# Optimization experiments

Measured on AMD Instinct MI355X. Metric: run time of the kernel, lower is better.

The kernel has to match this reference:

```python
import jax, jax.numpy as jnp
import numpy as np

N = 50000      # nodes
E = 1600000    # edges (before self loops)
B = 512        # graphs
D = 128        # gcn dim (constant across the 3 GAT layers)
H = 1024       # hidden_dim
O = 128        # output_dim
NEG_SLOPE = 0.2


def setup_inputs() -> dict:
    key = jax.random.key(0)
    ks = jax.random.split(key, 24)
    inp = {
        "x": jax.random.normal(ks[0], (N, D), jnp.float32),
        "edge_index": jax.random.randint(ks[1], (2, E), 0, N, dtype=jnp.int64),
        "edge_weight": jax.random.uniform(ks[2], (E,), jnp.float32),
        "batch": jnp.sort(jax.random.randint(ks[3], (N,), 0, B, dtype=jnp.int64)),
    }
    s = 1.0 / np.sqrt(D)
    for i in range(3):
        k = 4 + 4 * i
        inp[f"W{i+1}"] = jax.random.normal(ks[k], (D, D), jnp.float32) * s
        inp[f"as{i+1}"] = jax.random.normal(ks[k + 1], (D,), jnp.float32) * s
        inp[f"ad{i+1}"] = jax.random.normal(ks[k + 2], (D,), jnp.float32) * s
        inp[f"b{i+1}"] = jnp.zeros((D,), jnp.float32)
    inp["Wf1"] = jax.random.normal(ks[16], (D, H), jnp.float32) * s
    inp["bf1"] = jnp.zeros((H,), jnp.float32)
    inp["Wf2"] = jax.random.normal(ks[17], (H, O), jnp.float32) * (1.0 / np.sqrt(H))
    inp["bf2"] = jnp.zeros((O,), jnp.float32)
    return inp


def gat_conv(x, src, dst, W, a_src, a_dst, b):
    """PyG GATConv, heads=1: gather -> leakyrelu -> segment softmax -> scatter-add."""
    h = x @ W                                   # [N, D]
    e = jax.nn.leaky_relu(jnp.take(h @ a_src, src) + jnp.take(h @ a_dst, dst), NEG_SLOPE)  # [E']
    m = jax.ops.segment_max(e, dst, num_segments=N)
    ex = jnp.exp(e - m[dst])
    denom = jax.ops.segment_sum(ex, dst, num_segments=N)
    alpha = ex / denom[dst]                      # segment softmax over incoming edges
    out = jax.ops.segment_sum(alpha[:, None] * h[src], dst, num_segments=N)
    return out + b


def reference(x, edge_index, edge_weight, batch,
              W1, as1, ad1, b1, W2, as2, ad2, b2, W3, as3, ad3, b3,
              Wf1, bf1, Wf2, bf2):
    # GATConv adds self loops; edge_weight is unused by GATConv (faithful to original)
    loop = jnp.arange(N, dtype=edge_index.dtype)
    src = jnp.concatenate([edge_index[0], loop])
    dst = jnp.concatenate([edge_index[1], loop])

    h = gat_conv(x, src, dst, W1, as1, ad1, b1)
    h = jax.nn.relu(gat_conv(h, src, dst, W2, as2, ad2, b2))
    h = jax.nn.relu(gat_conv(h, src, dst, W3, as3, ad3, b3))

    # global mean pool (gep)
    sums = jax.ops.segment_sum(h, batch, num_segments=B)        # [B, D]
    counts = jax.ops.segment_sum(jnp.ones((N,), h.dtype), batch, num_segments=B)
    pooled = sums / jnp.maximum(counts, 1.0)[:, None]

    # MLP head; dropout is identity at inference
    o = jax.nn.relu(pooled) @ Wf1 + bf1
    o = jax.nn.relu(o) @ Wf2 + bf2
    return o
```

## Files before the change

### kernel.cpp

```cpp
#include <hip/hip_runtime.h>
#include <cstdint>
#include <cstddef>

#define NEG_SLOPE 0.2f

typedef _Float16 f16x8 __attribute__((ext_vector_type(8)));
typedef float f32x4v __attribute__((ext_vector_type(4)));

__device__ __forceinline__ unsigned enc_f(float f) {
  unsigned u = __float_as_uint(f);
  return (u & 0x80000000u) ? ~u : (u | 0x80000000u);
}
__device__ __forceinline__ float dec_f(unsigned u) {
  return (u & 0x80000000u) ? __uint_as_float(u ^ 0x80000000u) : __uint_as_float(~u);
}

#define AST 136
#define WST 136
#define HST 132
#define SMEM_BYTES (64 * AST * 2 + 128 * WST * 2)

__global__ void k_bounds(const int* __restrict__ batch, int N, int B,
                         int* __restrict__ gstart, unsigned* __restrict__ maxPart) {
  int n = blockIdx.x * blockDim.x + threadIdx.x;
  if (n < 768) maxPart[n] = 0u;
  if (n >= N) return;
  int cur = batch[n];
  if (n == 0) {
    for (int g = 0; g <= cur; g++) gstart[g] = 0;
  } else {
    int prev = batch[n - 1];
    for (int g = prev + 1; g <= cur; g++) gstart[g] = n;
  }
  if (n == N - 1) {
    for (int g = cur + 1; g <= B; g++) gstart[g] = N;
  }
}

__global__ void k_count_rank(const int* __restrict__ dst, int E,
                             int* counts, int* __restrict__ rank) {
  int e = blockIdx.x * blockDim.x + threadIdx.x;
  if (e < E) rank[e] = atomicAdd(&counts[dst[e]], 1);
}

__global__ __launch_bounds__(1024) void k_scan1(const int* __restrict__ counts, int N,
                                                int* __restrict__ row_ptr, int* __restrict__ part) {
  __shared__ int tmp[1024];
  int t = threadIdx.x;
  int i = blockIdx.x * 1024 + t;
  int v = (i < N) ? 1 + counts[i] : 0;
  tmp[t] = v;
  __syncthreads();
  for (int off = 1; off < 1024; off <<= 1) {
    int u = (t >= off) ? tmp[t - off] : 0;
    __syncthreads();
    tmp[t] += u;
    __syncthreads();
  }
  if (i < N) row_ptr[i + 1] = tmp[t];
  if (t == 1023) part[blockIdx.x] = tmp[t];
}

__global__ __launch_bounds__(1024) void k_scan3(int* __restrict__ row_ptr,
                                                const int* __restrict__ part, int N) {
  __shared__ int s_off;
  int bi = blockIdx.x;
  if (threadIdx.x == 0) {
    int run = 0;
    for (int b = 0; b < bi; b++) run += part[b];
    s_off = run;
    if (bi == 0) row_ptr[0] = 0;
  }
  __syncthreads();
  int i = bi * 1024 + threadIdx.x;
  if (i < N) row_ptr[i + 1] += s_off;
}

__global__ void k_fill(const int* __restrict__ src, const int* __restrict__ dst,
                       const int* __restrict__ rank, int E, int N,
                       const int* __restrict__ row_ptr, int* __restrict__ col) {
  int i = blockIdx.x * blockDim.x + threadIdx.x;
  if (i < N) col[row_ptr[i]] = i;
  int e = i - N;
  if (e >= 0 && e < E) col[row_ptr[dst[e]] + 1 + rank[e]] = src[e];
}

__global__ __launch_bounds__(256) void k_gemm_fused(const float* __restrict__ A32,
                                                    const unsigned short* __restrict__ A16,
                                                    const float* __restrict__ W,
                                                    unsigned short* __restrict__ hb,
                                                    const float* __restrict__ asrc,
                                                    const float* __restrict__ adst,
                                                    float* __restrict__ sv, float* __restrict__ dv,
                                                    unsigned* __restrict__ maxSlot, int M) {
  __shared__ __align__(16) char smem[SMEM_BYTES];
  __shared__ float redmax[4];
  _Float16* Ah = (_Float16*)smem;
  _Float16* Wt = (_Float16*)(smem + 64 * AST * 2);
  float*    hS = (float*)(smem + 64 * AST * 2);
  int t = threadIdx.x;
  int rowbase = blockIdx.x * 64;

  if (A16) {
    for (int i = t; i < 64 * 16; i += 256) {
      int r = i >> 4, c8 = (i & 15) << 3;
      int gr = rowbase + r;
      uint4 v = make_uint4(0u, 0u, 0u, 0u);
      if (gr < M) v = *(const uint4*)&A16[(size_t)gr * 128 + c8];
      *(uint4*)&Ah[r * AST + c8] = v;
    }
  } else {
    for (int i = t; i < 64 * 32; i += 256) {
      int r = i >> 5, c4 = (i & 31) << 2;
      int gr = rowbase + r;
      float4 v = make_float4(0.f, 0.f, 0.f, 0.f);
      if (gr < M) v = *(const float4*)&A32[(size_t)gr * 128 + c4];
      _Float16 tmp[4] = {(_Float16)v.x, (_Float16)v.y, (_Float16)v.z, (_Float16)v.w};
      *(short4*)&Ah[r * AST + c4] = *(short4*)tmp;
    }
  }
  for (int i = t; i < 128 * 32; i += 256) {
    int r = i >> 5, c4 = (i & 31) << 2;
    float4 v = *(const float4*)&W[(size_t)r * 128 + c4];
    Wt[(c4 + 0) * WST + r] = (_Float16)v.x;
    Wt[(c4 + 1) * WST + r] = (_Float16)v.y;
    Wt[(c4 + 2) * WST + r] = (_Float16)v.z;
    Wt[(c4 + 3) * WST + r] = (_Float16)v.w;
  }
  __syncthreads();

  int wave = t >> 6, lane = t & 63, quad = lane >> 4, l15 = lane & 15;
  f32x4v acc[4][2];
#pragma unroll
  for (int mt = 0; mt < 4; mt++)
#pragma unroll
    for (int nt = 0; nt < 2; nt++) {
      acc[mt][nt][0] = 0.f; acc[mt][nt][1] = 0.f; acc[mt][nt][2] = 0.f; acc[mt][nt][3] = 0.f;
    }

#pragma unroll
  for (int s = 0; s < 4; s++) {
    int k0 = (s << 5) + (quad << 3);
    f16x8 af[4], bf[2];
#pragma unroll
    for (int mt = 0; mt < 4; mt++)
      af[mt] = *(f16x8*)&Ah[(mt * 16 + l15) * AST + k0];
#pragma unroll
    for (int nt = 0; nt < 2; nt++)
      bf[nt] = *(f16x8*)&Wt[(wave * 32 + nt * 16 + l15) * WST + k0];
#pragma unroll
    for (int mt = 0; mt < 4; mt++)
#pragma unroll
      for (int nt = 0; nt < 2; nt++)
        acc[mt][nt] = __builtin_amdgcn_mfma_f32_16x16x32_f16(af[mt], bf[nt], acc[mt][nt], 0, 0, 0);
  }
  __syncthreads();

#pragma unroll
  for (int mt = 0; mt < 4; mt++)
#pragma unroll
    for (int nt = 0; nt < 2; nt++)
#pragma unroll
      for (int rr = 0; rr < 4; rr++)
        hS[(mt * 16 + quad * 4 + rr) * HST + wave * 32 + nt * 16 + l15] = acc[mt][nt][rr];
  __syncthreads();

  int tx = t & 31, ty = t >> 5;
  float4 av  = *(const float4*)&asrc[tx * 4];
  float4 adv = *(const float4*)&adst[tx * 4];
  float wmax = -1e30f;
#pragma unroll
  for (int r8 = 0; r8 < 8; r8++) {
    int row = r8 * 8 + ty;
    int gr = rowbase + row;
    float4 hv = *(float4*)&hS[row * HST + tx * 4];
    float ps = hv.x * av.x + hv.y * av.y + hv.z * av.z + hv.w * av.w;
    float pd = hv.x * adv.x + hv.y * adv.y + hv.z * adv.z + hv.w * adv.w;
#pragma unroll
    for (int mask = 16; mask; mask >>= 1) {
      ps += __shfl_xor(ps, mask);
      pd += __shfl_xor(pd, mask);
    }
    if (gr < M) {
      _Float16 hq[4] = {(_Float16)hv.x, (_Float16)hv.y, (_Float16)hv.z, (_Float16)hv.w};
      *(uint2*)&hb[(size_t)gr * 128 + tx * 4] = *(uint2*)hq;
      if (tx == 0) { sv[gr] = ps; dv[gr] = pd; wmax = fmaxf(wmax, ps); }
    }
  }
#pragma unroll
  for (int mask = 32; mask; mask >>= 1) wmax = fmaxf(wmax, __shfl_xor(wmax, mask));
  if ((t & 63) == 0) redmax[t >> 6] = wmax;
  __syncthreads();
  if (t == 0) {
    float mx = fmaxf(fmaxf(redmax[0], redmax[1]), fmaxf(redmax[2], redmax[3]));
    atomicMax(&maxSlot[blockIdx.x & 255], enc_f(mx));
  }
}

__global__ __launch_bounds__(256) void k_agg(const unsigned short* __restrict__ hb,
                                             const float* __restrict__ sv,
                                             const float* __restrict__ dv,
                                             const int* __restrict__ row_ptr,
                                             const int* __restrict__ col,
                                             const float* __restrict__ bias,
                                             const unsigned* __restrict__ maxSlot,
                                             unsigned short* __restrict__ out16,
                                             int N, int relu) {
  int wid = (int)((blockIdx.x * (size_t)blockDim.x + threadIdx.x) >> 6);
  int lane = threadIdx.x & 63;
  if (wid >= N) return;

  unsigned mp = max(max(maxSlot[lane], maxSlot[lane + 64]),
                    max(maxSlot[lane + 128], maxSlot[lane + 192]));
#pragma unroll
  for (int off = 32; off; off >>= 1) mp = max(mp, __shfl_xor(mp, off));
  float maxS = dec_f(mp);

  int beg = row_ptr[wid], end = row_ptr[wid + 1];
  float dn = dv[wid];
  float m = maxS + dn;
  m = (m > 0.f) ? m : NEG_SLOPE * m;

  int g = lane >> 4, sub = lane & 15;
  const uint32_t* hbu = (const uint32_t*)hb;
  float acc[8];
#pragma unroll
  for (int k = 0; k < 8; k++) acc[k] = 0.f;
  float dsum = 0.f;

  int j = beg + g;
  float wc = 0.f;
  uint4 hc = make_uint4(0u, 0u, 0u, 0u);
  if (j < end) {
    int sn = col[j];
    float e = sv[sn] + dn;
    e = (e > 0.f) ? e : NEG_SLOPE * e;
    wc = __expf(e - m);
    hc = *(const uint4*)(hbu + (size_t)sn * 64 + sub * 4);
  }
  j += 4;
  while (j < end) {
    int sn = col[j];
    float e = sv[sn] + dn;
    e = (e > 0.f) ? e : NEG_SLOPE * e;
    float wn = __expf(e - m);
    uint4 hn = *(const uint4*)(hbu + (size_t)sn * 64 + sub * 4);
    dsum += wc;
    const _Float16* hp = (const _Float16*)&hc;
#pragma unroll
    for (int k = 0; k < 8; k++) acc[k] += wc * (float)hp[k];
    wc = wn; hc = hn;
    j += 4;
  }
  {
    dsum += wc;
    const _Float16* hp = (const _Float16*)&hc;
#pragma unroll
    for (int k = 0; k < 8; k++) acc[k] += wc * (float)hp[k];
  }

  dsum += __shfl_xor(dsum, 16);
  dsum += __shfl_xor(dsum, 32);
#pragma unroll
  for (int k = 0; k < 8; k++) {
    acc[k] += __shfl_xor(acc[k], 16);
    acc[k] += __shfl_xor(acc[k], 32);
  }
  if (lane < 16) {
    float inv = 1.f / dsum;
    float o[8];
    const float* bp = &bias[sub * 8];
#pragma unroll
    for (int k = 0; k < 8; k++) {
      o[k] = acc[k] * inv + bp[k];
      if (relu) o[k] = fmaxf(o[k], 0.f);
    }
    _Float16 q[8];
#pragma unroll
    for (int k = 0; k < 8; k++) q[k] = (_Float16)o[k];
    *(uint4*)&out16[(size_t)wid * 128 + sub * 8] = *(uint4*)q;
  }
}

__global__ __launch_bounds__(64) void k_pool(const unsigned short* __restrict__ h16,
                                             const int* __restrict__ gstart,
                                             float* __restrict__ pooled, int B) {
  int b = blockIdx.x, c = threadIdx.x;
  int s0 = gstart[b], s1 = gstart[b + 1];
  const uint32_t* hu = (const uint32_t*)h16;
  float a0 = 0.f, a1 = 0.f;
  for (int n = s0; n < s1; n++) {
    union { uint32_t u; _Float16 h[2]; } cv;
    cv.u = hu[(size_t)n * 64 + c];
    a0 += (float)cv.h[0];
    a1 += (float)cv.h[1];
  }
  int cnt = s1 - s0;
  float inv = 1.f / (float)(cnt > 0 ? cnt : 1);
  pooled[b * 128 + 2 * c]     = fmaxf(a0 * inv, 0.f);
  pooled[b * 128 + 2 * c + 1] = fmaxf(a1 * inv, 0.f);
}

__global__ __launch_bounds__(256) void k_mlp(const float* __restrict__ pooled,
                                             const float* __restrict__ Wf1,
                                             const float* __restrict__ bf1,
                                             const float* __restrict__ Wf2,
                                             const float* __restrict__ bf2,
                                             float* __restrict__ out, int B) {
  __shared__ float P[4][128];
  __shared__ float H1[4][1024];
  __shared__ float R[4][128];
  int t = threadIdx.x;
  int g0 = blockIdx.x * 4;

  for (int i = t; i < 4 * 128; i += 256) {
    int gi = i >> 7, c = i & 127;
    P[gi][c] = (g0 + gi < B) ? pooled[(size_t)(g0 + gi) * 128 + c] : 0.f;
  }
  __syncthreads();

#pragma unroll
  for (int cb = 0; cb < 4; cb++) {
    int c = cb * 256 + t;
    float a0 = 0.f, a1 = 0.f, a2 = 0.f, a3 = 0.f;
    for (int k = 0; k < 128; k++) {
      float w = Wf1[(size_t)k * 1024 + c];
      a0 += P[0][k] * w; a1 += P[1][k] * w; a2 += P[2][k] * w; a3 += P[3][k] * w;
    }
    float b = bf1[c];
    H1[0][c] = fmaxf(a0 + b, 0.f);
    H1[1][c] = fmaxf(a1 + b, 0.f);
    H1[2][c] = fmaxf(a2 + b, 0.f);
    H1[3][c] = fmaxf(a3 + b, 0.f);
  }
  __syncthreads();

  int c = t & 127, hh = t >> 7;
  float a0 = 0.f, a1 = 0.f, a2 = 0.f, a3 = 0.f;
  int k0 = hh * 512;
  for (int k = k0; k < k0 + 512; k++) {
    float w = Wf2[(size_t)k * 128 + c];
    a0 += H1[0][k] * w; a1 += H1[1][k] * w; a2 += H1[2][k] * w; a3 += H1[3][k] * w;
  }
  if (hh == 1) { R[0][c] = a0; R[1][c] = a1; R[2][c] = a2; R[3][c] = a3; }
  __syncthreads();
  if (hh == 0) {
    float b = bf2[c];
    float o0 = a0 + R[0][c] + b;
    float o1 = a1 + R[1][c] + b;
    float o2 = a2 + R[2][c] + b;
    float o3 = a3 + R[3][c] + b;
    if (g0 + 0 < B) out[(size_t)(g0 + 0) * 128 + c] = o0;
    if (g0 + 1 < B) out[(size_t)(g0 + 1) * 128 + c] = o1;
    if (g0 + 2 < B) out[(size_t)(g0 + 2) * 128 + c] = o2;
    if (g0 + 3 < B) out[(size_t)(g0 + 3) * 128 + c] = o3;
  }
}

extern "C" void kernel_launch(void* const* d_in, const int* in_sizes, int n_in,
                              void* d_out, int out_size, void* d_ws, size_t ws_size,
                              hipStream_t stream) {
  const float* x     = (const float*)d_in[0];
  const int*   ei    = (const int*)d_in[1];
  const int*   batch = (const int*)d_in[3];
  const float* W1 = (const float*)d_in[4];
  const float* as1 = (const float*)d_in[5];
  const float* ad1 = (const float*)d_in[6];
  const float* b1 = (const float*)d_in[7];
  const float* W2 = (const float*)d_in[8];
  const float* as2 = (const float*)d_in[9];
  const float* ad2 = (const float*)d_in[10];
  const float* b2 = (const float*)d_in[11];
  const float* W3 = (const float*)d_in[12];
  const float* as3 = (const float*)d_in[13];
  const float* ad3 = (const float*)d_in[14];
  const float* b3 = (const float*)d_in[15];
  const float* Wf1 = (const float*)d_in[16];
  const float* bf1 = (const float*)d_in[17];
  const float* Wf2 = (const float*)d_in[18];
  const float* bf2 = (const float*)d_in[19];

  const int N = in_sizes[0] / 128;
  const int E = in_sizes[1] / 2;
  const int B = out_size / 128;

  char* base_ws = (char*)d_ws;
  size_t off = 0;
  auto carve = [&](size_t bytes) -> void* {
    off = (off + 255) & ~(size_t)255;
    void* p = base_ws + off;
    off += bytes;
    return p;
  };
  int* counts   = (int*)carve((size_t)N * 4);
  int* row_ptr  = (int*)carve((size_t)(N + 1) * 4);
  int* rank     = (int*)carve((size_t)E * 4);
  int* col      = (int*)carve((size_t)(E + N) * 4);
  int* part     = (int*)carve(1024 * 4);
  int* gstart   = (int*)carve((size_t)(B + 1) * 4);
  unsigned* maxPart = (unsigned*)carve(768 * 4);
  float* sbuf   = (float*)carve((size_t)N * 4);
  float* dbuf   = (float*)carve((size_t)N * 4);
  unsigned short* hb  = (unsigned short*)carve((size_t)N * 128 * 2);
  unsigned short* a16 = (unsigned short*)carve((size_t)N * 128 * 2);
  float* pooled = (float*)carve((size_t)B * 128 * 4);

  const int* srcp = ei;
  const int* dstp = ei + E;
  const int nb = (N + 1023) / 1024;
  const int Gg = (N + 63) / 64;

  hipMemsetAsync(counts, 0, (size_t)N * 4, stream);
  hipLaunchKernelGGL(k_bounds, dim3((N + 255) / 256), dim3(256), 0, stream,
                     batch, N, B, gstart, maxPart);
  hipLaunchKernelGGL(k_count_rank, dim3((E + 255) / 256), dim3(256), 0, stream,
                     dstp, E, counts, rank);
  hipLaunchKernelGGL(k_scan1, dim3(nb), dim3(1024), 0, stream, counts, N, row_ptr, part);
  hipLaunchKernelGGL(k_scan3, dim3(nb), dim3(1024), 0, stream, row_ptr, part, N);
  hipLaunchKernelGGL(k_fill, dim3((E + N + 255) / 256), dim3(256), 0, stream,
                     srcp, dstp, rank, E, N, row_ptr, col);

  hipLaunchKernelGGL(k_gemm_fused, dim3(Gg), dim3(256), 0, stream,
                     x, (const unsigned short*)nullptr, W1, hb, as1, ad1,
                     sbuf, dbuf, maxPart + 0 * 256, N);
  hipLaunchKernelGGL(k_agg, dim3((N + 3) / 4), dim3(256), 0, stream,
                     hb, sbuf, dbuf, row_ptr, col, b1, maxPart + 0 * 256, a16, N, 0);

  hipLaunchKernelGGL(k_gemm_fused, dim3(Gg), dim3(256), 0, stream,
                     (const float*)nullptr, a16, W2, hb, as2, ad2,
                     sbuf, dbuf, maxPart + 1 * 256, N);
  hipLaunchKernelGGL(k_agg, dim3((N + 3) / 4), dim3(256), 0, stream,
                     hb, sbuf, dbuf, row_ptr, col, b2, maxPart + 1 * 256, a16, N, 1);

  hipLaunchKernelGGL(k_gemm_fused, dim3(Gg), dim3(256), 0, stream,
                     (const float*)nullptr, a16, W3, hb, as3, ad3,
                     sbuf, dbuf, maxPart + 2 * 256, N);
  hipLaunchKernelGGL(k_agg, dim3((N + 3) / 4), dim3(256), 0, stream,
                     hb, sbuf, dbuf, row_ptr, col, b3, maxPart + 2 * 256, a16, N, 1);

  hipLaunchKernelGGL(k_pool, dim3(B), dim3(64), 0, stream, a16, gstart, pooled, B);
  hipLaunchKernelGGL(k_mlp, dim3((B + 3) / 4), dim3(256), 0, stream,
                     pooled, Wf1, bf1, Wf2, bf2, (float*)d_out, B);
}
```

Measured before the change: 558.2 us.

## Fuse CSR fill with first GEMM, fold count memset, parallelize pooling

Merges the CSR column fill and the layer-1 projection GEMM into one launch, interleaving one GEMM block among every nine blocks so the two independent workloads overlap. The zeroing of per-node counts moves into the bounds kernel, which removes a separate memset. The pooling kernel now uses four waves per graph that each sum a slice of the nodes, then combines them through shared memory. Together these cut launch count and serialization, at the cost of the fused kernel carrying the GEMM's large shared-memory allocation even for fill blocks, which may lower occupancy for the fill work.

```diff
diff --git a/kernel.cpp b/kernel.cpp
--- a/kernel.cpp
+++ b/kernel.cpp
@@ -21,10 +21,12 @@
 #define SMEM_BYTES (64 * AST * 2 + 128 * WST * 2)
 
 __global__ void k_bounds(const int* __restrict__ batch, int N, int B,
-                         int* __restrict__ gstart, unsigned* __restrict__ maxPart) {
+                         int* __restrict__ gstart, unsigned* __restrict__ maxPart,
+                         int* __restrict__ counts) {
   int n = blockIdx.x * blockDim.x + threadIdx.x;
   if (n < 768) maxPart[n] = 0u;
   if (n >= N) return;
+  counts[n] = 0;
   int cur = batch[n];
   if (n == 0) {
     for (int g = 0; g <= cur; g++) gstart[g] = 0;
@@ -76,17 +78,146 @@
   if (i < N) row_ptr[i + 1] += s_off;
 }
 
-__global__ void k_fill(const int* __restrict__ src, const int* __restrict__ dst,
-                       const int* __restrict__ rank, int E, int N,
-                       const int* __restrict__ row_ptr, int* __restrict__ col) {
-  int i = blockIdx.x * blockDim.x + threadIdx.x;
-  if (i < N) col[row_ptr[i]] = i;
-  int e = i - N;
-  if (e >= 0 && e < E) col[row_ptr[dst[e]] + 1 + rank[e]] = src[e];
-}
-
-__global__ __launch_bounds__(256) void k_gemm_fused(const float* __restrict__ A32,
-                                                    const unsigned short* __restrict__ A16,
+__device__ __forceinline__ void gemm_body(char* smem, float* redmax, int bx,
+                                          const float* __restrict__ A32,
+                                          const unsigned short* __restrict__ A16,
+                                          const float* __restrict__ W,
+                                          unsigned short* __restrict__ hb,
+                                          const float* __restrict__ asrc,
+                                          const float* __restrict__ adst,
+                                          float* __restrict__ sv, float* __restrict__ dv,
+                                          unsigned* __restrict__ maxSlot, int M) {
+  _Float16* Ah = (_Float16*)smem;
+  _Float16* Wt = (_Float16*)(smem + 64 * AST * 2);
+  float*    hS = (float*)(smem + 64 * AST * 2);
+  int t = threadIdx.x;
+  int rowbase = bx * 64;
+
+  if (A16) {
+    for (int i = t; i < 64 * 16; i += 256) {
+      int r = i >> 4, c8 = (i & 15) << 3;
+      int gr = rowbase + r;
+      uint4 v = make_uint4(0u, 0u, 0u, 0u);
+      if (gr < M) v = *(const uint4*)&A16[(size_t)gr * 128 + c8];
+      *(uint4*)&Ah[r * AST + c8] = v;
+    }
+  } else {
+    for (int i = t; i < 64 * 32; i += 256) {
+      int r = i >> 5, c4 = (i & 31) << 2;
+      int gr = rowbase + r;
+      float4 v = make_float4(0.f, 0.f, 0.f, 0.f);
+      if (gr < M) v = *(const float4*)&A32[(size_t)gr * 128 + c4];
+      _Float16 tmp[4] = {(_Float16)v.x, (_Float16)v.y, (_Float16)v.z, (_Float16)v.w};
+      *(short4*)&Ah[r * AST + c4] = *(short4*)tmp;
+    }
+  }
+  for (int i = t; i < 128 * 32; i += 256) {
+    int r = i >> 5, c4 = (i & 31) << 2;
+    float4 v = *(const float4*)&W[(size_t)r * 128 + c4];
+    Wt[(c4 + 0) * WST + r] = (_Float16)v.x;
+    Wt[(c4 + 1) * WST + r] = (_Float16)v.y;
+    Wt[(c4 + 2) * WST + r] = (_Float16)v.z;
+    Wt[(c4 + 3) * WST + r] = (_Float16)v.w;
+  }
+  __syncthreads();
+
+  int wave = t >> 6, lane = t & 63, quad = lane >> 4, l15 = lane & 15;
+  f32x4v acc[4][2];
+#pragma unroll
+  for (int mt = 0; mt < 4; mt++)
+#pragma unroll
+    for (int nt = 0; nt < 2; nt++) {
+      acc[mt][nt][0] = 0.f; acc[mt][nt][1] = 0.f; acc[mt][nt][2] = 0.f; acc[mt][nt][3] = 0.f;
+    }
+
+#pragma unroll
+  for (int s = 0; s < 4; s++) {
+    int k0 = (s << 5) + (quad << 3);
+    f16x8 af[4], bf[2];
+#pragma unroll
+    for (int mt = 0; mt < 4; mt++)
+      af[mt] = *(f16x8*)&Ah[(mt * 16 + l15) * AST + k0];
+#pragma unroll
+    for (int nt = 0; nt < 2; nt++)
+      bf[nt] = *(f16x8*)&Wt[(wave * 32 + nt * 16 + l15) * WST + k0];
+#pragma unroll
+    for (int mt = 0; mt < 4; mt++)
+#pragma unroll
+      for (int nt = 0; nt < 2; nt++)
+        acc[mt][nt] = __builtin_amdgcn_mfma_f32_16x16x32_f16(af[mt], bf[nt], acc[mt][nt], 0, 0, 0);
+  }
+  __syncthreads();
+
+#pragma unroll
+  for (int mt = 0; mt < 4; mt++)
+#pragma unroll
+    for (int nt = 0; nt < 2; nt++)
+#pragma unroll
+      for (int rr = 0; rr < 4; rr++)
+        hS[(mt * 16 + quad * 4 + rr) * HST + wave * 32 + nt * 16 + l15] = acc[mt][nt][rr];
+  __syncthreads();
+
+  int tx = t & 31, ty = t >> 5;
+  float4 av  = *(const float4*)&asrc[tx * 4];
+  float4 adv = *(const float4*)&adst[tx * 4];
+  float wmax = -1e30f;
+#pragma unroll
+  for (int r8 = 0; r8 < 8; r8++) {
+    int row = r8 * 8 + ty;
+    int gr = rowbase + row;
+    float4 hv = *(float4*)&hS[row * HST + tx * 4];
+    float ps = hv.x * av.x + hv.y * av.y + hv.z * av.z + hv.w * av.w;
+    float pd = hv.x * adv.x + hv.y * adv.y + hv.z * adv.z + hv.w * adv.w;
+#pragma unroll
+    for (int mask = 16; mask; mask >>= 1) {
+      ps += __shfl_xor(ps, mask);
+      pd += __shfl_xor(pd, mask);
+    }
+    if (gr < M) {
+      _Float16 hq[4] = {(_Float16)hv.x, (_Float16)hv.y, (_Float16)hv.z, (_Float16)hv.w};
+      *(uint2*)&hb[(size_t)gr * 128 + tx * 4] = *(uint2*)hq;
+      if (tx == 0) { sv[gr] = ps; dv[gr] = pd; wmax = fmaxf(wmax, ps); }
+    }
+  }
+#pragma unroll
+  for (int mask = 32; mask; mask >>= 1) wmax = fmaxf(wmax, __shfl_xor(wmax, mask));
+  if ((t & 63) == 0) redmax[t >> 6] = wmax;
+  __syncthreads();
+  if (t == 0) {
+    float mx = fmaxf(fmaxf(redmax[0], redmax[1]), fmaxf(redmax[2], redmax[3]));
+    atomicMax(&maxSlot[bx & 255], enc_f(mx));
+  }
+}
+
+__global__ __launch_bounds__(256) void k_fill_gemm(const int* __restrict__ src,
+                                                   const int* __restrict__ dst,
+                                                   const int* __restrict__ rank, int E, int N,
+                                                   const int* __restrict__ row_ptr,
+                                                   int* __restrict__ col,
+                                                   const float* __restrict__ A32,
+                                                   const float* __restrict__ W,
+                                                   unsigned short* __restrict__ hb,
+                                                   const float* __restrict__ asrc,
+                                                   const float* __restrict__ adst,
+                                                   float* __restrict__ sv, float* __restrict__ dv,
+                                                   unsigned* __restrict__ maxSlot, int Gg) {
+  __shared__ __align__(16) char smem[SMEM_BYTES];
+  __shared__ float redmax[4];
+  int b = (int)blockIdx.x;
+  bool isGemm = ((b % 9) == 4) && ((b / 9) < Gg);
+  if (isGemm) {
+    gemm_body(smem, redmax, b / 9, A32, (const unsigned short*)nullptr, W,
+              hb, asrc, adst, sv, dv, maxSlot, N);
+  } else {
+    int nGemmBefore = (b >= 4) ? min((b - 4) / 9 + 1, Gg) : 0;
+    int i = (b - nGemmBefore) * 256 + threadIdx.x;
+    if (i < N) col[row_ptr[i]] = i;
+    int e = i - N;
+    if (e >= 0 && e < E) col[row_ptr[dst[e]] + 1 + rank[e]] = src[e];
+  }
+}
+
+__global__ __launch_bounds__(256) void k_gemm_fused(const unsigned short* __restrict__ A16,
                                                     const float* __restrict__ W,
                                                     unsigned short* __restrict__ hb,
                                                     const float* __restrict__ asrc,
@@ -95,106 +226,8 @@
                                                     unsigned* __restrict__ maxSlot, int M) {
   __shared__ __align__(16) char smem[SMEM_BYTES];
   __shared__ float redmax[4];
-  _Float16* Ah = (_Float16*)smem;
-  _Float16* Wt = (_Float16*)(smem + 64 * AST * 2);
-  float*    hS = (float*)(smem + 64 * AST * 2);
-  int t = threadIdx.x;
-  int rowbase = blockIdx.x * 64;
-
-  if (A16) {
-    for (int i = t; i < 64 * 16; i += 256) {
-      int r = i >> 4, c8 = (i & 15) << 3;
-      int gr = rowbase + r;
-      uint4 v = make_uint4(0u, 0u, 0u, 0u);
-      if (gr < M) v = *(const uint4*)&A16[(size_t)gr * 128 + c8];
-      *(uint4*)&Ah[r * AST + c8] = v;
-    }
-  } else {
-    for (int i = t; i < 64 * 32; i += 256) {
-      int r = i >> 5, c4 = (i & 31) << 2;
-      int gr = rowbase + r;
-      float4 v = make_float4(0.f, 0.f, 0.f, 0.f);
-      if (gr < M) v = *(const float4*)&A32[(size_t)gr * 128 + c4];
-      _Float16 tmp[4] = {(_Float16)v.x, (_Float16)v.y, (_Float16)v.z, (_Float16)v.w};
-      *(short4*)&Ah[r * AST + c4] = *(short4*)tmp;
-    }
-  }
-  for (int i = t; i < 128 * 32; i += 256) {
-    int r = i >> 5, c4 = (i & 31) << 2;
-    float4 v = *(const float4*)&W[(size_t)r * 128 + c4];
-    Wt[(c4 + 0) * WST + r] = (_Float16)v.x;
-    Wt[(c4 + 1) * WST + r] = (_Float16)v.y;
-    Wt[(c4 + 2) * WST + r] = (_Float16)v.z;
-    Wt[(c4 + 3) * WST + r] = (_Float16)v.w;
-  }
-  __syncthreads();
-
-  int wave = t >> 6, lane = t & 63, quad = lane >> 4, l15 = lane & 15;
-  f32x4v acc[4][2];
-#pragma unroll
-  for (int mt = 0; mt < 4; mt++)
-#pragma unroll
-    for (int nt = 0; nt < 2; nt++) {
-      acc[mt][nt][0] = 0.f; acc[mt][nt][1] = 0.f; acc[mt][nt][2] = 0.f; acc[mt][nt][3] = 0.f;
-    }
-
-#pragma unroll
-  for (int s = 0; s < 4; s++) {
-    int k0 = (s << 5) + (quad << 3);
-    f16x8 af[4], bf[2];
-#pragma unroll
-    for (int mt = 0; mt < 4; mt++)
-      af[mt] = *(f16x8*)&Ah[(mt * 16 + l15) * AST + k0];
-#pragma unroll
-    for (int nt = 0; nt < 2; nt++)
-      bf[nt] = *(f16x8*)&Wt[(wave * 32 + nt * 16 + l15) * WST + k0];
-#pragma unroll
-    for (int mt = 0; mt < 4; mt++)
-#pragma unroll
-      for (int nt = 0; nt < 2; nt++)
-        acc[mt][nt] = __builtin_amdgcn_mfma_f32_16x16x32_f16(af[mt], bf[nt], acc[mt][nt], 0, 0, 0);
-  }
-  __syncthreads();
-
-#pragma unroll
-  for (int mt = 0; mt < 4; mt++)
-#pragma unroll
-    for (int nt = 0; nt < 2; nt++)
-#pragma unroll
-      for (int rr = 0; rr < 4; rr++)
-        hS[(mt * 16 + quad * 4 + rr) * HST + wave * 32 + nt * 16 + l15] = acc[mt][nt][rr];
-  __syncthreads();
-
-  int tx = t & 31, ty = t >> 5;
-  float4 av  = *(const float4*)&asrc[tx * 4];
-  float4 adv = *(const float4*)&adst[tx * 4];
-  float wmax = -1e30f;
-#pragma unroll
-  for (int r8 = 0; r8 < 8; r8++) {
-    int row = r8 * 8 + ty;
-    int gr = rowbase + row;
-    float4 hv = *(float4*)&hS[row * HST + tx * 4];
-    float ps = hv.x * av.x + hv.y * av.y + hv.z * av.z + hv.w * av.w;
-    float pd = hv.x * adv.x + hv.y * adv.y + hv.z * adv.z + hv.w * adv.w;
-#pragma unroll
-    for (int mask = 16; mask; mask >>= 1) {
-      ps += __shfl_xor(ps, mask);
-      pd += __shfl_xor(pd, mask);
-    }
-    if (gr < M) {
-      _Float16 hq[4] = {(_Float16)hv.x, (_Float16)hv.y, (_Float16)hv.z, (_Float16)hv.w};
-      *(uint2*)&hb[(size_t)gr * 128 + tx * 4] = *(uint2*)hq;
-      if (tx == 0) { sv[gr] = ps; dv[gr] = pd; wmax = fmaxf(wmax, ps); }
-    }
-  }
-#pragma unroll
-  for (int mask = 32; mask; mask >>= 1) wmax = fmaxf(wmax, __shfl_xor(wmax, mask));
-  if ((t & 63) == 0) redmax[t >> 6] = wmax;
-  __syncthreads();
-  if (t == 0) {
-    float mx = fmaxf(fmaxf(redmax[0], redmax[1]), fmaxf(redmax[2], redmax[3]));
-    atomicMax(&maxSlot[blockIdx.x & 255], enc_f(mx));
-  }
+  gemm_body(smem, redmax, (int)blockIdx.x, (const float*)nullptr, A16, W,
+            hb, asrc, adst, sv, dv, maxSlot, M);
 }
 
 __global__ __launch_bounds__(256) void k_agg(const unsigned short* __restrict__ hb,
@@ -282,23 +315,34 @@
   }
 }
 
-__global__ __launch_bounds__(64) void k_pool(const unsigned short* __restrict__ h16,
-                                             const int* __restrict__ gstart,
-                                             float* __restrict__ pooled, int B) {
-  int b = blockIdx.x, c = threadIdx.x;
+__global__ __launch_bounds__(256) void k_pool(const unsigned short* __restrict__ h16,
+                                              const int* __restrict__ gstart,
+                                              float* __restrict__ pooled, int B) {
+  __shared__ float red[4][128];
+  int b = blockIdx.x, t = threadIdx.x;
+  int c = t & 63, seg = t >> 6;
   int s0 = gstart[b], s1 = gstart[b + 1];
+  int cnt = s1 - s0;
+  int per = (cnt + 3) >> 2;
+  int n0 = s0 + seg * per;
+  int n1 = min(n0 + per, s1);
   const uint32_t* hu = (const uint32_t*)h16;
   float a0 = 0.f, a1 = 0.f;
-  for (int n = s0; n < s1; n++) {
+  for (int n = n0; n < n1; n++) {
     union { uint32_t u; _Float16 h[2]; } cv;
     cv.u = hu[(size_t)n * 64 + c];
     a0 += (float)cv.h[0];
     a1 += (float)cv.h[1];
   }
-  int cnt = s1 - s0;
-  float inv = 1.f / (float)(cnt > 0 ? cnt : 1);
-  pooled[b * 128 + 2 * c]     = fmaxf(a0 * inv, 0.f);
-  pooled[b * 128 + 2 * c + 1] = fmaxf(a1 * inv, 0.f);
+  if (seg) { red[seg][2 * c] = a0; red[seg][2 * c + 1] = a1; }
+  __syncthreads();
+  if (seg == 0) {
+    a0 += red[1][2 * c] + red[2][2 * c] + red[3][2 * c];
+    a1 += red[1][2 * c + 1] + red[2][2 * c + 1] + red[3][2 * c + 1];
+    float inv = 1.f / (float)(cnt > 0 ? cnt : 1);
+    pooled[b * 128 + 2 * c]     = fmaxf(a0 * inv, 0.f);
+    pooled[b * 128 + 2 * c + 1] = fmaxf(a1 * inv, 0.f);
+  }
 }
 
 __global__ __launch_bounds__(256) void k_mlp(const float* __restrict__ pooled,
@@ -409,36 +453,33 @@
   const int* dstp = ei + E;
   const int nb = (N + 1023) / 1024;
   const int Gg = (N + 63) / 64;
-
-  hipMemsetAsync(counts, 0, (size_t)N * 4, stream);
+  const int Gf = (E + N + 255) / 256;
+
   hipLaunchKernelGGL(k_bounds, dim3((N + 255) / 256), dim3(256), 0, stream,
-                     batch, N, B, gstart, maxPart);
+                     batch, N, B, gstart, maxPart, counts);
   hipLaunchKernelGGL(k_count_rank, dim3((E + 255) / 256), dim3(256), 0, stream,
                      dstp, E, counts, rank);
   hipLaunchKernelGGL(k_scan1, dim3(nb), dim3(1024), 0, stream, counts, N, row_ptr, part);
   hipLaunchKernelGGL(k_scan3, dim3(nb), dim3(1024), 0, stream, row_ptr, part, N);
-  hipLaunchKernelGGL(k_fill, dim3((E + N + 255) / 256), dim3(256), 0, stream,
-                     srcp, dstp, rank, E, N, row_ptr, col);
-
-  hipLaunchKernelGGL(k_gemm_fused, dim3(Gg), dim3(256), 0, stream,
-                     x, (const unsigned short*)nullptr, W1, hb, as1, ad1,
-                     sbuf, dbuf, maxPart + 0 * 256, N);
+
+  hipLaunchKernelGGL(k_fill_gemm, dim3(Gf + Gg), dim3(256), 0, stream,
+                     srcp, dstp, rank, E, N, row_ptr, col,
+                     x, W1, hb, as1, ad1, sbuf, dbuf, maxPart + 0 * 256, Gg);
+
   hipLaunchKernelGGL(k_agg, dim3((N + 3) / 4), dim3(256), 0, stream,
                      hb, sbuf, dbuf, row_ptr, col, b1, maxPart + 0 * 256, a16, N, 0);
 
   hipLaunchKernelGGL(k_gemm_fused, dim3(Gg), dim3(256), 0, stream,
-                     (const float*)nullptr, a16, W2, hb, as2, ad2,
-                     sbuf, dbuf, maxPart + 1 * 256, N);
+                     a16, W2, hb, as2, ad2, sbuf, dbuf, maxPart + 1 * 256, N);
   hipLaunchKernelGGL(k_agg, dim3((N + 3) / 4), dim3(256), 0, stream,
                      hb, sbuf, dbuf, row_ptr, col, b2, maxPart + 1 * 256, a16, N, 1);
 
   hipLaunchKernelGGL(k_gemm_fused, dim3(Gg), dim3(256), 0, stream,
-                     (const float*)nullptr, a16, W3, hb, as3, ad3,
-                     sbuf, dbuf, maxPart + 2 * 256, N);
+                     a16, W3, hb, as3, ad3, sbuf, dbuf, maxPart + 2 * 256, N);
   hipLaunchKernelGGL(k_agg, dim3((N + 3) / 4), dim3(256), 0, stream,
                      hb, sbuf, dbuf, row_ptr, col, b3, maxPart + 2 * 256, a16, N, 1);
 
-  hipLaunchKernelGGL(k_pool, dim3(B), dim3(64), 0, stream, a16, gstart, pooled, B);
+  hipLaunchKernelGGL(k_pool, dim3(B), dim3(256), 0, stream, a16, gstart, pooled, B);
   hipLaunchKernelGGL(k_mlp, dim3((B + 3) / 4), dim3(256), 0, stream,
                      pooled, Wf1, bf1, Wf2, bf2, (float*)d_out, B);
 }
```

New measurement: 532.4 us. 4.6% less time.
